# Performance work log

Hardware: AMD Instinct MI355X
Metric: run time of the kernel (lower is better)

Reference implementation:

```python
import jax, jax.numpy as jnp
import numpy as np
from jax import lax

MAX_DISP = 4  # patch_size = 2*MAX_DISP+1 = 9; kernel_size=1, stride=1, padding=0


def setup_inputs() -> dict:
    key = jax.random.key(0)
    k1, k2 = jax.random.split(key)
    B, C, H, W = 4, 256, 96, 96
    feat1 = jax.random.normal(k1, (B, C, H, W), dtype=jnp.float32)
    feat2 = jax.random.normal(k2, (B, C, H, W), dtype=jnp.float32)
    return {"feat1": feat1, "feat2": feat2}


def _cost_volume(feat1, feat2):
    # SpatialCorrelationSampler with kernel_size=1, patch_size=2*MAX_DISP+1,
    # stride=1, padding=0: for each displacement (dy,dx) in [-d,d]^2,
    # corr[b,dy,dx,y,x] = sum_c feat1[b,c,y,x] * feat2[b,c,y+dy,x+dx]
    # (out-of-bounds feat2 treated as zero). Output reshaped to [B, P*P, H, W].
    B, C, H, W = feat1.shape
    d = MAX_DISP
    P = 2 * d + 1
    f2_pad = jnp.pad(feat2, ((0, 0), (0, 0), (d, d), (d, d)))
    # flattened displacement offsets into the padded map, shape [P*P, 2]
    dy, dx = jnp.meshgrid(jnp.arange(P), jnp.arange(P), indexing="ij")
    offsets = jnp.stack([dy.ravel(), dx.ravel()], axis=-1)  # [P*P, 2]

    def step(carry, off):
        f2 = lax.dynamic_slice(f2_pad, (0, 0, off[0], off[1]), (B, C, H, W))
        corr = jnp.einsum("bchw,bchw->bhw", feat1, f2)  # sum over channels
        return carry, corr

    _, cv = lax.scan(step, None, offsets)  # [P*P, B, H, W]
    return jnp.transpose(cv, (1, 0, 2, 3))  # [B, P*P, H, W]


def reference(feat1, feat2):
    return _cost_volume(feat1, feat2)
```

## Files before the change

kernel.cpp:

```cpp
#include <hip/hip_runtime.h>


typedef _Float16 f16x8 __attribute__((ext_vector_type(8)));
typedef float f32x4 __attribute__((ext_vector_type(4)));

#define NB 4
#define NC 256
#define NH 96
#define NW 96
#define NP 9
#define PLANE (NH * NW)
#define TENS (NB * NH * NW * NC)
#define WS_NEED (2ull * (unsigned long long)TENS * 2ull)
#define TPT (TENS / 8)
#define PACK_BLK (2 * TPT / 256)
#define MAIN_BLK 2304
#define CGSTR (NW * 8)
#define ROWSTR (32 * CGSTR)
#define LPAD 37

__global__ __launch_bounds__(256) void pack_t(const float* __restrict__ f1,
                                              const float* __restrict__ f2,
                                              _Float16* __restrict__ ws)
{
    const int e   = blockIdx.x * 256 + threadIdx.x;
    const int t   = e / TPT;
    const int r   = e % TPT;
    const int row = r / (NW * 32);
    const int q   = r % (NW * 32);
    const int x   = q % NW;
    const int cg  = q / NW;
    const int b   = row / NH;
    const int y   = row % NH;

    const float* s  = t ? f2 : f1;
    const float* sp = s + ((size_t)(b * NC + cg * 8) * NH + y) * NW + x;
    f16x8 o;
#pragma unroll
    for (int j = 0; j < 8; ++j) o[j] = (_Float16)sp[(size_t)j * PLANE];
    *(f16x8*)(ws + (size_t)t * TENS + ((size_t)row * 32 + cg) * CGSTR + (size_t)x * 8) = o;
}

__global__ __launch_bounds__(192) void costvol_mfma(const _Float16* __restrict__ ws,
                                                    float* __restrict__ out)
{
    __shared__ float lds[81][20];

    const _Float16* f1p = ws;
    const _Float16* f2p = ws + (size_t)TENS;

    const int bid = blockIdx.x;
    const int swz = (bid & 7) * (MAIN_BLK / 8) + (bid >> 3);
    const int mt  = swz % 6;
    const int y   = (swz / 6) % 96;
    const int b   = swz / 576;

    const int w    = threadIdx.x >> 6;
    const int lane = threadIdx.x & 63;
    const int lr   = lane & 15;
    const int lg   = lane >> 4;
    const int m0   = mt * 16;

    const _Float16* pa = f1p + ((size_t)(b * 96 + y) * 32 + lg) * CGSTR + (size_t)(m0 + lr) * 8;
    f16x8 a[8];
#pragma unroll
    for (int ks = 0; ks < 8; ++ks) a[ks] = *(const f16x8*)(pa + (size_t)ks * 4 * CGSTR);

    const int n0a = m0 - 8 + lr;
    const int n0b = m0 + 8 + lr;
    const bool inA = (n0a >= 0);
    const bool inB = (n0b < 96);
    const f16x8 bz = {};

#pragma unroll
    for (int i = 0; i < 3; ++i) {
        const int dy = w * 3 + i;
        const int y2 = y + dy - 4;
        f32x4 acc0 = {0.f, 0.f, 0.f, 0.f};
        f32x4 acc1 = {0.f, 0.f, 0.f, 0.f};

        if (y2 >= 0 && y2 < 96) {
            const _Float16* base = f2p + (size_t)(b * 96 + y2) * ROWSTR + (size_t)lg * CGSTR;
            const _Float16* pba  = base + (ptrdiff_t)n0a * 8;
            const _Float16* pbb  = base + (ptrdiff_t)n0b * 8;
#pragma unroll
            for (int ks = 0; ks < 8; ++ks) {
                f16x8 b0 = bz, b1 = bz;
                if (inA) b0 = *(const f16x8*)(pba + (size_t)ks * 4 * CGSTR);
                if (inB) b1 = *(const f16x8*)(pbb + (size_t)ks * 4 * CGSTR);
                acc0 = __builtin_amdgcn_mfma_f32_16x16x32_f16(a[ks], b0, acc0, 0, 0, 0);
                acc1 = __builtin_amdgcn_mfma_f32_16x16x32_f16(a[ks], b1, acc1, 0, 0, 0);
            }
        }

#pragma unroll
        for (int reg = 0; reg < 4; ++reg) {
            const int mrow = lg * 4 + reg;
            const int dx0  = lr - mrow - 4;
            const int dx1  = dx0 + 16;
            if (dx0 >= 0 && dx0 <= 8) lds[dy * 9 + dx0][mrow] = acc0[reg];
            if (dx1 >= 0 && dx1 <= 8) lds[dy * 9 + dx1][mrow] = acc1[reg];
        }
    }

    __syncthreads();

    const int q = (threadIdx.x & 3) * 4;
#pragma unroll
    for (int r = threadIdx.x >> 2; r < 81; r += 48) {
        const float4 v = make_float4(lds[r][q], lds[r][q + 1],
                                     lds[r][q + 2], lds[r][q + 3]);
        *(float4*)(out + ((size_t)(b * 81 + r) * PLANE) + y * 96 + m0 + q) = v;
    }
}

__global__ __launch_bounds__(256) void costvol_f32(const float* __restrict__ f1,
                                                   const float* __restrict__ f2,
                                                   float* __restrict__ out)
{
    __shared__ float lds[2 * 64 * LPAD];
    const int bid = blockIdx.x;
    const int swz = (bid & 7) * (1296 / 8) + (bid >> 3);
    const int dyi = swz % NP;
    const int g   = swz / NP;
    const int w    = threadIdx.x >> 6;
    const int lane = threadIdx.x & 63;
    const int chk = g * 64 + lane;
    const int b   = chk / (NH * 24);
    const int rem = chk - b * (NH * 24);
    const int y   = rem / 24;
    const int x0  = (rem - y * 24) * 4;
    const int y2  = y + dyi - 4;

    float acc[NP][4];
#pragma unroll
    for (int i = 0; i < NP; ++i)
#pragma unroll
        for (int j = 0; j < 4; ++j) acc[i][j] = 0.f;

    if (y2 >= 0 && y2 < NH) {
        const float* p1 = f1 + ((size_t)(b * NC + w * 64) * NH + y) * NW + x0;
        const float* p2 = f2 + ((size_t)(b * NC + w * 64) * NH + y2) * NW + x0;
        const bool hasL = (x0 >= 4);
        const bool hasR = (x0 <= NW - 8);
#pragma unroll 4
        for (int c = 0; c < 64; ++c) {
            const float4 av = *(const float4*)p1;
            const float4 Lv = hasL ? *(const float4*)(p2 - 4) : make_float4(0.f, 0.f, 0.f, 0.f);
            const float4 Mv = *(const float4*)(p2);
            const float4 Rv = hasR ? *(const float4*)(p2 + 4) : make_float4(0.f, 0.f, 0.f, 0.f);
            const float wv[12] = {Lv.x, Lv.y, Lv.z, Lv.w, Mv.x, Mv.y, Mv.z, Mv.w,
                                  Rv.x, Rv.y, Rv.z, Rv.w};
            const float aa[4] = {av.x, av.y, av.z, av.w};
#pragma unroll
            for (int dxi = 0; dxi < NP; ++dxi)
#pragma unroll
                for (int j = 0; j < 4; ++j) acc[dxi][j] += aa[j] * wv[dxi + j];
            p1 += PLANE;
            p2 += PLANE;
        }
    }

    float* reg0 = &lds[0 * 64 * LPAD + lane * LPAD];
    float* reg1 = &lds[1 * 64 * LPAD + lane * LPAD];
    if (w >= 2) {
        float* dst = (w == 2) ? reg0 : reg1;
#pragma unroll
        for (int dxi = 0; dxi < NP; ++dxi)
#pragma unroll
            for (int j = 0; j < 4; ++j) dst[dxi * 4 + j] = acc[dxi][j];
    }
    __syncthreads();
    if (w < 2) {
        const float* src = (w == 0) ? reg0 : reg1;
#pragma unroll
        for (int dxi = 0; dxi < NP; ++dxi)
#pragma unroll
            for (int j = 0; j < 4; ++j) acc[dxi][j] += src[dxi * 4 + j];
    }
    __syncthreads();
    if (w == 1) {
#pragma unroll
        for (int dxi = 0; dxi < NP; ++dxi)
#pragma unroll
            for (int j = 0; j < 4; ++j) reg0[dxi * 4 + j] = acc[dxi][j];
    }
    __syncthreads();
    if (w == 0) {
#pragma unroll
        for (int dxi = 0; dxi < NP; ++dxi)
#pragma unroll
            for (int j = 0; j < 4; ++j) acc[dxi][j] += reg0[dxi * 4 + j];
        float* ob = out + ((size_t)(b * 81 + dyi * 9) * NH + y) * NW + x0;
#pragma unroll
        for (int dxi = 0; dxi < NP; ++dxi) {
            *(float4*)ob = make_float4(acc[dxi][0], acc[dxi][1], acc[dxi][2], acc[dxi][3]);
            ob += PLANE;
        }
    }
}

extern "C" void kernel_launch(void* const* d_in, const int* in_sizes, int n_in,
                              void* d_out, int out_size, void* d_ws, size_t ws_size,
                              hipStream_t stream) {
    const float* f1 = (const float*)d_in[0];
    const float* f2 = (const float*)d_in[1];
    float* out = (float*)d_out;
    if (ws_size >= WS_NEED) {
        _Float16* ws = (_Float16*)d_ws;
        pack_t<<<dim3(PACK_BLK, 1, 1), dim3(256, 1, 1), 0, stream>>>(f1, f2, ws);
        costvol_mfma<<<dim3(MAIN_BLK, 1, 1), dim3(192, 1, 1), 0, stream>>>(ws, out);
    } else {
        costvol_f32<<<dim3(1296, 1, 1), dim3(256, 1, 1), 0, stream>>>(f1, f2, out);
    }
}
```

Before: 44.97 us.

## Vectorize pack loads with float4 and batch B loads before MFMA chain

The pack kernel now reads four x positions per channel with float4 loads and writes four f16x8 vectors per thread, replacing scalar strided loads. This cuts load instruction count and the thread count by a factor of four. In the MFMA kernel, all eight B fragments for each dy are loaded into registers before the MFMA chain, which exposes more memory-level parallelism. The dy loop is also changed to unroll 1, which limits register growth but serializes the three dy iterations.

```diff
diff --git a/kernel.cpp b/kernel.cpp
--- a/kernel.cpp
+++ b/kernel.cpp
@@ -12,8 +12,8 @@
 #define PLANE (NH * NW)
 #define TENS (NB * NH * NW * NC)
 #define WS_NEED (2ull * (unsigned long long)TENS * 2ull)
-#define TPT (TENS / 8)
-#define PACK_BLK (2 * TPT / 256)
+#define TPT4 (TENS / 32)
+#define PACK_BLK (2 * TPT4 / 256)
 #define MAIN_BLK 2304
 #define CGSTR (NW * 8)
 #define ROWSTR (32 * CGSTR)
@@ -24,21 +24,32 @@
                                               _Float16* __restrict__ ws)
 {
     const int e   = blockIdx.x * 256 + threadIdx.x;
-    const int t   = e / TPT;
-    const int r   = e % TPT;
-    const int row = r / (NW * 32);
-    const int q   = r % (NW * 32);
-    const int x   = q % NW;
-    const int cg  = q / NW;
+    const int t   = e / TPT4;
+    const int r   = e % TPT4;
+    const int row = r / 768;
+    const int q   = r % 768;
+    const int cg  = q / 24;
+    const int x4  = q % 24;
     const int b   = row / NH;
     const int y   = row % NH;
 
     const float* s  = t ? f2 : f1;
-    const float* sp = s + ((size_t)(b * NC + cg * 8) * NH + y) * NW + x;
-    f16x8 o;
-#pragma unroll
-    for (int j = 0; j < 8; ++j) o[j] = (_Float16)sp[(size_t)j * PLANE];
-    *(f16x8*)(ws + (size_t)t * TENS + ((size_t)row * 32 + cg) * CGSTR + (size_t)x * 8) = o;
+    const float* sp = s + ((size_t)(b * NC + cg * 8) * NH + y) * NW + x4 * 4;
+    float vv[8][4];
+#pragma unroll
+    for (int j = 0; j < 8; ++j) {
+        const float4 v = *(const float4*)(sp + (size_t)j * PLANE);
+        vv[j][0] = v.x; vv[j][1] = v.y; vv[j][2] = v.z; vv[j][3] = v.w;
+    }
+    _Float16* dp = ws + (size_t)t * TENS + ((size_t)row * 32 + cg) * CGSTR
+                 + (size_t)x4 * 32;
+#pragma unroll
+    for (int xi = 0; xi < 4; ++xi) {
+        f16x8 o;
+#pragma unroll
+        for (int j = 0; j < 8; ++j) o[j] = (_Float16)vv[j][xi];
+        *(f16x8*)(dp + xi * 8) = o;
+    }
 }
 
 __global__ __launch_bounds__(192) void costvol_mfma(const _Float16* __restrict__ ws,
@@ -72,7 +83,7 @@
     const bool inB = (n0b < 96);
     const f16x8 bz = {};
 
-#pragma unroll
+#pragma unroll 1
     for (int i = 0; i < 3; ++i) {
         const int dy = w * 3 + i;
         const int y2 = y + dy - 4;
@@ -83,13 +94,16 @@
             const _Float16* base = f2p + (size_t)(b * 96 + y2) * ROWSTR + (size_t)lg * CGSTR;
             const _Float16* pba  = base + (ptrdiff_t)n0a * 8;
             const _Float16* pbb  = base + (ptrdiff_t)n0b * 8;
+            f16x8 B0[8], B1[8];
 #pragma unroll
             for (int ks = 0; ks < 8; ++ks) {
-                f16x8 b0 = bz, b1 = bz;
-                if (inA) b0 = *(const f16x8*)(pba + (size_t)ks * 4 * CGSTR);
-                if (inB) b1 = *(const f16x8*)(pbb + (size_t)ks * 4 * CGSTR);
-                acc0 = __builtin_amdgcn_mfma_f32_16x16x32_f16(a[ks], b0, acc0, 0, 0, 0);
-                acc1 = __builtin_amdgcn_mfma_f32_16x16x32_f16(a[ks], b1, acc1, 0, 0, 0);
+                B0[ks] = inA ? *(const f16x8*)(pba + (size_t)ks * 4 * CGSTR) : bz;
+                B1[ks] = inB ? *(const f16x8*)(pbb + (size_t)ks * 4 * CGSTR) : bz;
+            }
+#pragma unroll
+            for (int ks = 0; ks < 8; ++ks) {
+                acc0 = __builtin_amdgcn_mfma_f32_16x16x32_f16(a[ks], B0[ks], acc0, 0, 0, 0);
+                acc1 = __builtin_amdgcn_mfma_f32_16x16x32_f16(a[ks], B1[ks], acc1, 0, 0, 0);
             }
         }
 
```

After: 44.70 us. About the same (-0.6%).
